# Kernel optimization log

Measured on AMD Instinct MI355X. Metric: run time of the kernel, lower is better.

Reference implementation:

```python
import jax, jax.numpy as jnp
import numpy as np

HIDDEN = 2048
N_HEADS = 32
N_KV_HEADS = 8
HEAD_DIM = 64
MAX_SEQ_LEN = 4096
ROPE_THETA = 500000.0
B, L = 1, 2048
EPS = 1e-6
NEG = -1e9


def precompute_rope(head_dim, max_seq_len, theta):
    freqs = 1.0 / theta ** (jnp.arange(0, head_dim, 2, dtype=jnp.float32) / head_dim)
    pos = jnp.arange(max_seq_len, dtype=jnp.float32)
    ang = pos[:, None] * freqs[None, :]                     # [S, hd/2]
    cos = jnp.repeat(jnp.cos(ang), 2, axis=-1)              # [S, hd]
    sin = jnp.repeat(jnp.sin(ang), 2, axis=-1)
    return cos, sin


def apply_rope(x, cos, sin):
    # x: [B, H, L, hd]; interleaved (even/odd) rotation, faithful to torch code
    seq_len = x.shape[2]
    c = cos[:seq_len][None, None, :, ::2]                   # [1,1,L,hd/2]
    s = sin[:seq_len][None, None, :, ::2]
    x1 = x[..., ::2]
    x2 = x[..., 1::2]
    o1 = x1 * c - x2 * s
    o2 = x2 * c + x1 * s
    return jnp.stack([o1, o2], axis=-1).reshape(x.shape)


def rmsnorm(x, w):
    return x * jax.lax.rsqrt(jnp.mean(x * x, axis=-1, keepdims=True) + EPS) * w


def setup_inputs() -> dict:
    key = jax.random.key(0)
    ks = jax.random.split(key, 6)
    x = jax.random.normal(ks[0], (B, L, HIDDEN), dtype=jnp.float32)
    causal = jnp.tril(jnp.ones((L, L), dtype=bool))
    mask = jnp.where(causal, 0.0, NEG).astype(jnp.float32)  # additive causal mask
    scale = 0.02
    norm_w = jnp.ones((HIDDEN,), dtype=jnp.float32)
    Wq = jax.random.normal(ks[1], (N_HEADS * HEAD_DIM, HIDDEN), dtype=jnp.float32) * scale
    Wk = jax.random.normal(ks[2], (N_KV_HEADS * HEAD_DIM, HIDDEN), dtype=jnp.float32) * scale
    Wv = jax.random.normal(ks[3], (N_KV_HEADS * HEAD_DIM, HIDDEN), dtype=jnp.float32) * scale
    Wo = jax.random.normal(ks[4], (HIDDEN, N_HEADS * HEAD_DIM), dtype=jnp.float32) * scale
    rope_cos, rope_sin = precompute_rope(HEAD_DIM, MAX_SEQ_LEN, ROPE_THETA)
    return {"x": x, "mask": mask, "norm_w": norm_w, "Wq": Wq, "Wk": Wk,
            "Wv": Wv, "Wo": Wo, "rope_cos": rope_cos, "rope_sin": rope_sin}


def reference(x, mask, norm_w, Wq, Wk, Wv, Wo, rope_cos, rope_sin):
    Bb, Ll, _ = x.shape
    residual = x
    h = rmsnorm(x, norm_w)
    q = (h @ Wq.T).reshape(Bb, Ll, N_HEADS, HEAD_DIM).transpose(0, 2, 1, 3)     # [B,H,L,hd]
    k = (h @ Wk.T).reshape(Bb, Ll, N_KV_HEADS, HEAD_DIM).transpose(0, 2, 1, 3)  # [B,Hk,L,hd]
    v = (h @ Wv.T).reshape(Bb, Ll, N_KV_HEADS, HEAD_DIM).transpose(0, 2, 1, 3)
    q = apply_rope(q, rope_cos, rope_sin)
    k = apply_rope(k, rope_cos, rope_sin)
    n_groups = N_HEADS // N_KV_HEADS
    if n_groups > 1:
        k = jnp.repeat(k, n_groups, axis=1)   # GQA repeat_interleave
        v = jnp.repeat(v, n_groups, axis=1)
    scale = jnp.sqrt(jnp.asarray(HEAD_DIM, dtype=q.dtype))
    attn = jnp.einsum('bhld,bhmd->bhlm', q, k) / scale
    attn = attn + mask                                       # broadcast [L,L]
    attn = jax.nn.softmax(attn, axis=-1)
    out = jnp.einsum('bhlm,bhmd->bhld', attn, v)
    out = out.transpose(0, 2, 1, 3).reshape(Bb, Ll, N_HEADS * HEAD_DIM)
    return out @ Wo.T + residual
```

## Files before the change

### kernel.cpp

```cpp
#include <hip/hip_runtime.h>
#include <stdint.h>

#define L_SEQ 2048
#define HID   2048
#define NHEAD 32
#define NKV   8
#define HD    64
#define KVDIM 512
#define QSCALE 0.18033688f

typedef __attribute__((ext_vector_type(8))) short s16x8;
typedef __attribute__((ext_vector_type(4))) short s16x4;
typedef __attribute__((ext_vector_type(4))) float f32x4;

__device__ __forceinline__ short f2bf(float f) {
  __bf16 b = (__bf16)f;
  short s;
  __builtin_memcpy(&s, &b, 2);
  return s;
}

__device__ __forceinline__ void gload16(const void* g, void* l) {
  __builtin_amdgcn_global_load_lds(
      (const __attribute__((address_space(1))) void*)g,
      (__attribute__((address_space(3))) void*)l, 16, 0, 0);
}

__global__ __launch_bounds__(256) void pre_kernel(
    const float* __restrict__ x, const float* __restrict__ w,
    const float* __restrict__ wq, const float* __restrict__ wk,
    const float* __restrict__ wv, const float* __restrict__ wo,
    short* __restrict__ h,
    short* __restrict__ owq, short* __restrict__ owk,
    short* __restrict__ owv, short* __restrict__ owo) {
  const int tid = threadIdx.x;
  if (blockIdx.x >= 2048) {
    int64_t e = ((int64_t)(blockIdx.x - 2048) * 256 + tid) * 4;
    const float* src; short* dst; int64_t o;
    if (e < 4194304)      { src = wq; dst = owq; o = e; }
    else if (e < 5242880) { src = wk; dst = owk; o = e - 4194304; }
    else if (e < 6291456) { src = wv; dst = owv; o = e - 5242880; }
    else                  { src = wo; dst = owo; o = e - 6291456; }
    f32x4 v = *(const f32x4*)(src + o);
    s16x4 b;
    b[0] = f2bf(v[0]); b[1] = f2bf(v[1]); b[2] = f2bf(v[2]); b[3] = f2bf(v[3]);
    *(s16x4*)(dst + o) = b;
    return;
  }
  const int row = blockIdx.x;
  const float* xr = x + (int64_t)row * HID + tid * 8;
  f32x4 a = *(const f32x4*)(xr);
  f32x4 b = *(const f32x4*)(xr + 4);
  float ss = a[0]*a[0]+a[1]*a[1]+a[2]*a[2]+a[3]*a[3]
           + b[0]*b[0]+b[1]*b[1]+b[2]*b[2]+b[3]*b[3];
  #pragma unroll
  for (int off = 1; off < 64; off <<= 1) ss += __shfl_xor(ss, off, 64);
  __shared__ float sred[4];
  if ((tid & 63) == 0) sred[tid >> 6] = ss;
  __syncthreads();
  const float scale = rsqrtf((sred[0]+sred[1]+sred[2]+sred[3]) * (1.0f/HID) + 1e-6f);
  const float* wp = w + tid * 8;
  f32x4 wa = *(const f32x4*)(wp);
  f32x4 wb = *(const f32x4*)(wp + 4);
  s16x8 o;
  o[0]=f2bf(a[0]*scale*wa[0]); o[1]=f2bf(a[1]*scale*wa[1]);
  o[2]=f2bf(a[2]*scale*wa[2]); o[3]=f2bf(a[3]*scale*wa[3]);
  o[4]=f2bf(b[0]*scale*wb[0]); o[5]=f2bf(b[1]*scale*wb[1]);
  o[6]=f2bf(b[2]*scale*wb[2]); o[7]=f2bf(b[3]*scale*wb[3]);
  *(s16x8*)(h + (int64_t)row * HID + tid * 8) = o;
}

__device__ __forceinline__ void gemm_core_128x64(
    const short* __restrict__ A, const short* __restrict__ B,
    short* sA, short* sB, f32x4 acc[4][2]) {
  const int tid = threadIdx.x;
  const int lane = tid & 63;
  const int w = tid >> 6, wr = w >> 1, wc = w & 1;
  const int g = lane >> 4, li = lane & 15;

  auto stage = [&](int k0, int buf) {
    #pragma unroll
    for (int i = 0; i < 4; ++i) {
      const int flat = i * 256 + tid;
      const int row = flat >> 3, c8 = flat & 7;
      const int sc = c8 ^ (row & 7);
      gload16(A + (int64_t)row * HID + k0 + sc * 8, sA + buf * 8192 + flat * 8);
    }
    #pragma unroll
    for (int i = 0; i < 2; ++i) {
      const int flat = i * 256 + tid;
      const int row = flat >> 3, c8 = flat & 7;
      const int sc = c8 ^ (row & 7);
      gload16(B + (int64_t)row * HID + k0 + sc * 8, sB + buf * 4096 + flat * 8);
    }
  };

  stage(0, 0);
  for (int k0 = 0; k0 < HID; k0 += 64) {
    const int cur = (k0 >> 6) & 1;
    __syncthreads();
    if (k0 + 64 < HID) stage(k0 + 64, cur ^ 1);
    const short* cA = sA + cur * 8192;
    const short* cB = sB + cur * 4096;
    #pragma unroll
    for (int kk = 0; kk < 2; ++kk) {
      s16x8 af[4], bfr[2];
      const int chunk = (kk << 2) | g;
      #pragma unroll
      for (int m = 0; m < 4; ++m) {
        const int row = wr * 64 + m * 16 + li;
        af[m] = *(const s16x8*)(cA + row * 64 + ((chunk ^ (li & 7)) << 3));
      }
      #pragma unroll
      for (int n = 0; n < 2; ++n) {
        const int row = wc * 32 + n * 16 + li;
        bfr[n] = *(const s16x8*)(cB + row * 64 + ((chunk ^ (li & 7)) << 3));
      }
      __builtin_amdgcn_s_setprio(1);
      #pragma unroll
      for (int m = 0; m < 4; ++m)
        #pragma unroll
        for (int n = 0; n < 2; ++n)
          acc[m][n] = __builtin_amdgcn_mfma_f32_16x16x32_bf16(af[m], bfr[n], acc[m][n], 0, 0, 0);
      __builtin_amdgcn_s_setprio(0);
    }
  }
}

__global__ __launch_bounds__(256) void qkv_kernel(
    const short* __restrict__ h16, const short* __restrict__ wq,
    const short* __restrict__ wk, const short* __restrict__ wv,
    short* __restrict__ qo, short* __restrict__ ko, short* __restrict__ vto,
    const float* __restrict__ rc, const float* __restrict__ rs) {
  __shared__ short sA[2 * 128 * 64];
  __shared__ short sB[2 * 64 * 64];
  const int cb = blockIdx.x, rb = blockIdx.y;
  const short* B; short* out; int colbase, mode; int64_t ldc;
  if (cb < 32)      { B = wq + (int64_t)cb * 64 * HID;        out = qo;  colbase = cb * 64;        mode = 0; ldc = HID;   }
  else if (cb < 40) { B = wk + (int64_t)(cb - 32) * 64 * HID; out = ko;  colbase = (cb - 32) * 64; mode = 0; ldc = KVDIM; }
  else              { B = wv + (int64_t)(cb - 40) * 64 * HID; out = vto; colbase = (cb - 40) * 64; mode = 1; ldc = L_SEQ; }
  const float rsc = (cb < 32) ? QSCALE : 1.0f;

  f32x4 acc[4][2];
  const f32x4 z = {0.f, 0.f, 0.f, 0.f};
  #pragma unroll
  for (int m = 0; m < 4; ++m)
    #pragma unroll
    for (int n = 0; n < 2; ++n) acc[m][n] = z;

  gemm_core_128x64(h16 + (int64_t)rb * 128 * HID, B, sA, sB, acc);

  const int lane = threadIdx.x & 63;
  const int w = threadIdx.x >> 6, wr = w >> 1, wc = w & 1;
  const int g = lane >> 4, li = lane & 15;

  if (mode == 0) {
    #pragma unroll
    for (int m = 0; m < 4; ++m) {
      #pragma unroll
      for (int n = 0; n < 2; ++n) {
        const int col = colbase + wc * 32 + n * 16 + li;
        const int d2 = col & 62;
        #pragma unroll
        for (int r = 0; r < 4; ++r) {
          const int row = rb * 128 + wr * 64 + m * 16 + g * 4 + r;
          const float c = rc[row * 64 + d2] * rsc;
          const float s = rs[row * 64 + d2] * rsc;
          const float v0 = acc[m][n][r];
          const float pr = __shfl_xor(v0, 1, 64);
          const float o = (lane & 1) ? (v0 * c + pr * s) : (v0 * c - pr * s);
          out[(int64_t)row * ldc + col] = f2bf(o);
        }
      }
    }
  } else {
    #pragma unroll
    for (int m = 0; m < 4; ++m) {
      #pragma unroll
      for (int n = 0; n < 2; ++n) {
        const int col = colbase + wc * 32 + n * 16 + li;
        const int row0 = rb * 128 + wr * 64 + m * 16 + g * 4;
        s16x4 pk;
        pk[0] = f2bf(acc[m][n][0]); pk[1] = f2bf(acc[m][n][1]);
        pk[2] = f2bf(acc[m][n][2]); pk[3] = f2bf(acc[m][n][3]);
        *(s16x4*)(out + (int64_t)col * L_SEQ + row0) = pk;
      }
    }
  }
}

__global__ __launch_bounds__(512, 4) void attn_kernel(
    const short* __restrict__ q16, const short* __restrict__ k16,
    const short* __restrict__ vt16, short* __restrict__ out16) {
  __shared__ short sK[2 * 64 * 64];
  __shared__ short sV[2 * 64 * 64];
  __shared__ short sP[8][16 * 64];
  const int pi = blockIdx.x, h = blockIdx.y, kvh = h >> 2;
  const int qbL = pi, qbH = 31 - pi;
  const int tid = threadIdx.x, lane = tid & 63, w = tid >> 6, wl = w & 3;
  const int g = lane >> 4, li = lane & 15;
  const int myqb = (w < 4) ? qbL : qbH;
  short* sPw = &sP[w][0];

  s16x8 qf[2];
  {
    const int qr = myqb * 64 + wl * 16 + li;
    #pragma unroll
    for (int kk = 0; kk < 2; ++kk)
      qf[kk] = *(const s16x8*)(q16 + (int64_t)qr * HID + h * 64 + kk * 32 + g * 8);
  }

  f32x4 acc[4];
  const f32x4 z = {0.f, 0.f, 0.f, 0.f};
  #pragma unroll
  for (int n = 0; n < 4; ++n) acc[n] = z;
  float m = -1e30f, l = 0.f;

  auto stage = [&](int t, int buf) {
    const int kv0 = t * 64;
    const int row = tid >> 3, c8 = tid & 7;
    const int sc = c8 ^ (row & 7);
    gload16(k16 + (int64_t)(kv0 + row) * KVDIM + kvh * 64 + sc * 8,
            sK + buf * 4096 + tid * 8);
    gload16(vt16 + (int64_t)(kvh * 64 + row) * L_SEQ + kv0 + sc * 8,
            sV + buf * 4096 + tid * 8);
  };

  stage(0, 0);
  for (int t = 0; t <= qbH; ++t) {
    const int cur = t & 1;
    __syncthreads();
    if (t < qbH) stage(t + 1, cur ^ 1);
    if (w >= 4 || t <= qbL) {
      const short* cK = sK + cur * 4096;
      const short* cV = sV + cur * 4096;

      s16x8 kf[2][4];
      #pragma unroll
      for (int kk = 0; kk < 2; ++kk)
        #pragma unroll
        for (int n = 0; n < 4; ++n)
          kf[kk][n] = *(const s16x8*)(cK + (n * 16 + li) * 64 + ((((kk << 2) | g) ^ (li & 7)) << 3));
      f32x4 s[4];
      #pragma unroll
      for (int n = 0; n < 4; ++n) s[n] = z;
      __builtin_amdgcn_s_setprio(1);
      #pragma unroll
      for (int kk = 0; kk < 2; ++kk)
        #pragma unroll
        for (int n = 0; n < 4; ++n)
          s[n] = __builtin_amdgcn_mfma_f32_16x16x32_bf16(kf[kk][n], qf[kk], s[n], 0, 0, 0);
      __builtin_amdgcn_s_setprio(0);

      if (t == myqb) {
        const int ql = wl * 16 + li;
        #pragma unroll
        for (int n = 0; n < 4; ++n)
          #pragma unroll
          for (int r = 0; r < 4; ++r)
            if (n * 16 + g * 4 + r > ql) s[n][r] = -1e30f;
      }

      float mx = fmaxf(fmaxf(s[0][0], s[0][1]), fmaxf(s[0][2], s[0][3]));
      #pragma unroll
      for (int n = 1; n < 4; ++n)
        mx = fmaxf(mx, fmaxf(fmaxf(s[n][0], s[n][1]), fmaxf(s[n][2], s[n][3])));
      mx = fmaxf(mx, __shfl_xor(mx, 16, 64));
      mx = fmaxf(mx, __shfl_xor(mx, 32, 64));
      if (__any(mx > m + 8.0f)) {
        const float mn = fmaxf(m, mx);
        const float al = __builtin_amdgcn_exp2f(m - mn);
        m = mn;
        l *= al;
        #pragma unroll
        for (int dt = 0; dt < 4; ++dt)
          #pragma unroll
          for (int r = 0; r < 4; ++r) acc[dt][r] *= al;
      }
      float ps = 0.f;
      #pragma unroll
      for (int n = 0; n < 4; ++n) {
        s16x4 pk;
        #pragma unroll
        for (int r = 0; r < 4; ++r) {
          const float p = __builtin_amdgcn_exp2f(s[n][r] - m);
          pk[r] = f2bf(p);
          ps += p;
        }
        *(s16x4*)(sPw + li * 64 + (((n * 2 + (g >> 1)) ^ (li & 7)) << 3) + (g & 1) * 4) = pk;
      }
      ps += __shfl_xor(ps, 16, 64);
      ps += __shfl_xor(ps, 32, 64);
      l += ps;

      s16x8 vf[2][4];
      #pragma unroll
      for (int kk = 0; kk < 2; ++kk)
        #pragma unroll
        for (int dt = 0; dt < 4; ++dt)
          vf[kk][dt] = *(const s16x8*)(cV + (dt * 16 + li) * 64 + ((((kk << 2) | g) ^ (li & 7)) << 3));
      #pragma unroll
      for (int kk = 0; kk < 2; ++kk) {
        s16x8 pf = *(const s16x8*)(sPw + li * 64 + (((kk * 4 + g) ^ (li & 7)) << 3));
        __builtin_amdgcn_s_setprio(1);
        #pragma unroll
        for (int dt = 0; dt < 4; ++dt)
          acc[dt] = __builtin_amdgcn_mfma_f32_16x16x32_bf16(vf[kk][dt], pf, acc[dt], 0, 0, 0);
        __builtin_amdgcn_s_setprio(0);
      }
    }
  }

  const float rl = 1.0f / l;
  #pragma unroll
  for (int n2 = 0; n2 < 4; ++n2) {
    s16x4 o;
    #pragma unroll
    for (int r = 0; r < 4; ++r) o[r] = f2bf(acc[n2][r] * rl);
    *(s16x4*)(sPw + li * 64 + (((n2 * 2 + (g >> 1)) ^ (li & 7)) << 3) + (g & 1) * 4) = o;
  }
  #pragma unroll
  for (int half = 0; half < 2; ++half) {
    const int chunk = half * 64 + lane;
    const int q = chunk >> 3, c = chunk & 7;
    s16x8 v = *(const s16x8*)(sPw + q * 64 + ((c ^ (q & 7)) << 3));
    *(s16x8*)(out16 + (int64_t)(myqb * 64 + wl * 16 + q) * HID + h * 64 + c * 8) = v;
  }
}

__global__ __launch_bounds__(256) void oproj_kernel(
    const short* __restrict__ ao, const short* __restrict__ wo,
    const float* __restrict__ resid, float* __restrict__ out) {
  __shared__ short sA[2 * 128 * 64];
  __shared__ short sB[2 * 64 * 64];
  const int cb = blockIdx.x, rb = blockIdx.y;
  f32x4 acc[4][2];
  const f32x4 z = {0.f, 0.f, 0.f, 0.f};
  #pragma unroll
  for (int m = 0; m < 4; ++m)
    #pragma unroll
    for (int n = 0; n < 2; ++n) acc[m][n] = z;

  gemm_core_128x64(ao + (int64_t)rb * 128 * HID, wo + (int64_t)cb * 64 * HID, sA, sB, acc);

  const int lane = threadIdx.x & 63;
  const int w = threadIdx.x >> 6, wr = w >> 1, wc = w & 1;
  const int g = lane >> 4, li = lane & 15;
  #pragma unroll
  for (int m = 0; m < 4; ++m) {
    #pragma unroll
    for (int n = 0; n < 2; ++n) {
      const int col = cb * 64 + wc * 32 + n * 16 + li;
      #pragma unroll
      for (int r = 0; r < 4; ++r) {
        const int row = rb * 128 + wr * 64 + m * 16 + g * 4 + r;
        out[(int64_t)row * HID + col] = acc[m][n][r] + resid[(int64_t)row * HID + col];
      }
    }
  }
}

extern "C" void kernel_launch(void* const* d_in, const int* in_sizes, int n_in,
                              void* d_out, int out_size, void* d_ws, size_t ws_size,
                              hipStream_t stream) {
  (void)in_sizes; (void)n_in; (void)out_size; (void)ws_size;
  const float* x      = (const float*)d_in[0];
  const float* norm_w = (const float*)d_in[2];
  const float* Wq     = (const float*)d_in[3];
  const float* Wk     = (const float*)d_in[4];
  const float* Wv     = (const float*)d_in[5];
  const float* Wo     = (const float*)d_in[6];
  const float* rc     = (const float*)d_in[7];
  const float* rs     = (const float*)d_in[8];
  float* out = (float*)d_out;

  char* ws = (char*)d_ws;
  short* wq16 = (short*)(ws);
  short* wk16 = (short*)(ws + 8388608);
  short* wv16 = (short*)(ws + 10485760);
  short* wo16 = (short*)(ws + 12582912);
  short* h16  = (short*)(ws + 20971520);
  short* q16  = (short*)(ws + 29360128);
  short* k16  = (short*)(ws + 37748736);
  short* vt16 = (short*)(ws + 39845888);
  short* ao16 = (short*)(ws + 41943040);

  pre_kernel<<<12288, 256, 0, stream>>>(x, norm_w, Wq, Wk, Wv, Wo,
                                        h16, wq16, wk16, wv16, wo16);
  qkv_kernel<<<dim3(48, 16), 256, 0, stream>>>(h16, wq16, wk16, wv16, q16, k16, vt16, rc, rs);
  attn_kernel<<<dim3(16, NHEAD), 512, 0, stream>>>(q16, k16, vt16, ao16);
  oproj_kernel<<<dim3(32, 16), 256, 0, stream>>>(ao16, wo16, x, out);
}
```

Baseline: 127.3 us.

## Process four query blocks per attention workgroup to reuse staged K/V tiles

Each attention workgroup now handles four causal query blocks (two per wave group: kb/31-kb and 8+kb/23-kb) instead of two, and the grid is halved to 8x32. Each K/V tile staged into LDS and loaded into registers is shared by two query blocks per wave, which cuts LDS staging and global K/V traffic per unit of work. In exchange there are half as many workgroups (256 on a large GPU), more registers per wave for the extra accumulators and Q fragments, and possible load imbalance between the two wave groups.

```diff
diff --git a/kernel.cpp b/kernel.cpp
--- a/kernel.cpp
+++ b/kernel.cpp
@@ -189,32 +189,111 @@
   }
 }
 
+__device__ __forceinline__ void softmax_pv(
+    f32x4 s[4], const s16x8 vf[2][4], bool diag,
+    int w, int g, int li, short* sPw,
+    float& m, float& l, f32x4 acc[4]) {
+  if (diag) {
+    const int ql = w * 16 + li;
+    #pragma unroll
+    for (int n = 0; n < 4; ++n)
+      #pragma unroll
+      for (int r = 0; r < 4; ++r)
+        if (n * 16 + g * 4 + r > ql) s[n][r] = -1e30f;
+  }
+  float mx = fmaxf(fmaxf(s[0][0], s[0][1]), fmaxf(s[0][2], s[0][3]));
+  #pragma unroll
+  for (int n = 1; n < 4; ++n)
+    mx = fmaxf(mx, fmaxf(fmaxf(s[n][0], s[n][1]), fmaxf(s[n][2], s[n][3])));
+  mx = fmaxf(mx, __shfl_xor(mx, 16, 64));
+  mx = fmaxf(mx, __shfl_xor(mx, 32, 64));
+  if (__any(mx > m + 8.0f)) {
+    const float mn = fmaxf(m, mx);
+    const float al = __builtin_amdgcn_exp2f(m - mn);
+    m = mn;
+    l *= al;
+    #pragma unroll
+    for (int dt = 0; dt < 4; ++dt)
+      #pragma unroll
+      for (int r = 0; r < 4; ++r) acc[dt][r] *= al;
+  }
+  float ps = 0.f;
+  #pragma unroll
+  for (int n = 0; n < 4; ++n) {
+    s16x4 pk;
+    #pragma unroll
+    for (int r = 0; r < 4; ++r) {
+      const float p = __builtin_amdgcn_exp2f(s[n][r] - m);
+      pk[r] = f2bf(p);
+      ps += p;
+    }
+    *(s16x4*)(sPw + li * 64 + (((n * 2 + (g >> 1)) ^ (li & 7)) << 3) + (g & 1) * 4) = pk;
+  }
+  ps += __shfl_xor(ps, 16, 64);
+  ps += __shfl_xor(ps, 32, 64);
+  l += ps;
+  #pragma unroll
+  for (int kk = 0; kk < 2; ++kk) {
+    s16x8 pf = *(const s16x8*)(sPw + li * 64 + (((kk * 4 + g) ^ (li & 7)) << 3));
+    __builtin_amdgcn_s_setprio(1);
+    #pragma unroll
+    for (int dt = 0; dt < 4; ++dt)
+      acc[dt] = __builtin_amdgcn_mfma_f32_16x16x32_bf16(vf[kk][dt], pf, acc[dt], 0, 0, 0);
+    __builtin_amdgcn_s_setprio(0);
+  }
+}
+
+__device__ __forceinline__ void write_out(
+    const f32x4 acc[4], float l, int qb, int h, int w, int g, int li, int lane,
+    short* sPw, short* __restrict__ out16) {
+  const float rl = 1.0f / l;
+  #pragma unroll
+  for (int n2 = 0; n2 < 4; ++n2) {
+    s16x4 o;
+    #pragma unroll
+    for (int r = 0; r < 4; ++r) o[r] = f2bf(acc[n2][r] * rl);
+    *(s16x4*)(sPw + li * 64 + (((n2 * 2 + (g >> 1)) ^ (li & 7)) << 3) + (g & 1) * 4) = o;
+  }
+  #pragma unroll
+  for (int half = 0; half < 2; ++half) {
+    const int chunk = half * 64 + lane;
+    const int q = chunk >> 3, c = chunk & 7;
+    s16x8 v = *(const s16x8*)(sPw + q * 64 + ((c ^ (q & 7)) << 3));
+    *(s16x8*)(out16 + (int64_t)(qb * 64 + w * 16 + q) * HID + h * 64 + c * 8) = v;
+  }
+}
+
 __global__ __launch_bounds__(512, 4) void attn_kernel(
     const short* __restrict__ q16, const short* __restrict__ k16,
     const short* __restrict__ vt16, short* __restrict__ out16) {
   __shared__ short sK[2 * 64 * 64];
   __shared__ short sV[2 * 64 * 64];
   __shared__ short sP[8][16 * 64];
-  const int pi = blockIdx.x, h = blockIdx.y, kvh = h >> 2;
-  const int qbL = pi, qbH = 31 - pi;
+  const int kb = blockIdx.x;
+  const int h = blockIdx.y, kvh = h >> 2;
   const int tid = threadIdx.x, lane = tid & 63, w = tid >> 6, wl = w & 3;
   const int g = lane >> 4, li = lane & 15;
-  const int myqb = (w < 4) ? qbL : qbH;
+  const int myqbL = (w < 4) ? kb : 8 + kb;
+  const int myqbH = (w < 4) ? 31 - kb : 23 - kb;
+  const int tmax = 31 - kb;
   short* sPw = &sP[w][0];
 
-  s16x8 qf[2];
+  s16x8 qfL[2], qfH[2];
   {
-    const int qr = myqb * 64 + wl * 16 + li;
-    #pragma unroll
-    for (int kk = 0; kk < 2; ++kk)
-      qf[kk] = *(const s16x8*)(q16 + (int64_t)qr * HID + h * 64 + kk * 32 + g * 8);
-  }
-
-  f32x4 acc[4];
+    const int qrL = myqbL * 64 + wl * 16 + li;
+    const int qrH = myqbH * 64 + wl * 16 + li;
+    #pragma unroll
+    for (int kk = 0; kk < 2; ++kk) {
+      qfL[kk] = *(const s16x8*)(q16 + (int64_t)qrL * HID + h * 64 + kk * 32 + g * 8);
+      qfH[kk] = *(const s16x8*)(q16 + (int64_t)qrH * HID + h * 64 + kk * 32 + g * 8);
+    }
+  }
+
+  f32x4 accL[4], accH[4];
   const f32x4 z = {0.f, 0.f, 0.f, 0.f};
   #pragma unroll
-  for (int n = 0; n < 4; ++n) acc[n] = z;
-  float m = -1e30f, l = 0.f;
+  for (int n = 0; n < 4; ++n) { accL[n] = z; accH[n] = z; }
+  float mL = -1e30f, lL = 0.f, mH = -1e30f, lH = 0.f;
 
   auto stage = [&](int t, int buf) {
     const int kv0 = t * 64;
@@ -227,11 +306,13 @@
   };
 
   stage(0, 0);
-  for (int t = 0; t <= qbH; ++t) {
+  for (int t = 0; t <= tmax; ++t) {
     const int cur = t & 1;
     __syncthreads();
-    if (t < qbH) stage(t + 1, cur ^ 1);
-    if (w >= 4 || t <= qbL) {
+    if (t < tmax) stage(t + 1, cur ^ 1);
+    const bool doH = (t <= myqbH);
+    const bool doL = (t <= myqbL);
+    if (doH) {
       const short* cK = sK + cur * 4096;
       const short* cV = sV + cur * 4096;
 
@@ -241,57 +322,28 @@
         #pragma unroll
         for (int n = 0; n < 4; ++n)
           kf[kk][n] = *(const s16x8*)(cK + (n * 16 + li) * 64 + ((((kk << 2) | g) ^ (li & 7)) << 3));
-      f32x4 s[4];
-      #pragma unroll
-      for (int n = 0; n < 4; ++n) s[n] = z;
+
+      f32x4 sH[4], sL[4];
+      #pragma unroll
+      for (int n = 0; n < 4; ++n) sH[n] = z;
       __builtin_amdgcn_s_setprio(1);
       #pragma unroll
       for (int kk = 0; kk < 2; ++kk)
         #pragma unroll
         for (int n = 0; n < 4; ++n)
-          s[n] = __builtin_amdgcn_mfma_f32_16x16x32_bf16(kf[kk][n], qf[kk], s[n], 0, 0, 0);
+          sH[n] = __builtin_amdgcn_mfma_f32_16x16x32_bf16(kf[kk][n], qfH[kk], sH[n], 0, 0, 0);
       __builtin_amdgcn_s_setprio(0);
-
-      if (t == myqb) {
-        const int ql = wl * 16 + li;
-        #pragma unroll
-        for (int n = 0; n < 4; ++n)
+      if (doL) {
+        #pragma unroll
+        for (int n = 0; n < 4; ++n) sL[n] = z;
+        __builtin_amdgcn_s_setprio(1);
+        #pragma unroll
+        for (int kk = 0; kk < 2; ++kk)
           #pragma unroll
-          for (int r = 0; r < 4; ++r)
-            if (n * 16 + g * 4 + r > ql) s[n][r] = -1e30f;
-      }
-
-      float mx = fmaxf(fmaxf(s[0][0], s[0][1]), fmaxf(s[0][2], s[0][3]));
-      #pragma unroll
-      for (int n = 1; n < 4; ++n)
-        mx = fmaxf(mx, fmaxf(fmaxf(s[n][0], s[n][1]), fmaxf(s[n][2], s[n][3])));
-      mx = fmaxf(mx, __shfl_xor(mx, 16, 64));
-      mx = fmaxf(mx, __shfl_xor(mx, 32, 64));
-      if (__any(mx > m + 8.0f)) {
-        const float mn = fmaxf(m, mx);
-        const float al = __builtin_amdgcn_exp2f(m - mn);
-        m = mn;
-        l *= al;
-        #pragma unroll
-        for (int dt = 0; dt < 4; ++dt)
-          #pragma unroll
-          for (int r = 0; r < 4; ++r) acc[dt][r] *= al;
-      }
-      float ps = 0.f;
-      #pragma unroll
-      for (int n = 0; n < 4; ++n) {
-        s16x4 pk;
-        #pragma unroll
-        for (int r = 0; r < 4; ++r) {
-          const float p = __builtin_amdgcn_exp2f(s[n][r] - m);
-          pk[r] = f2bf(p);
-          ps += p;
-        }
-        *(s16x4*)(sPw + li * 64 + (((n * 2 + (g >> 1)) ^ (li & 7)) << 3) + (g & 1) * 4) = pk;
-      }
-      ps += __shfl_xor(ps, 16, 64);
-      ps += __shfl_xor(ps, 32, 64);
-      l += ps;
+          for (int n = 0; n < 4; ++n)
+            sL[n] = __builtin_amdgcn_mfma_f32_16x16x32_bf16(kf[kk][n], qfL[kk], sL[n], 0, 0, 0);
+        __builtin_amdgcn_s_setprio(0);
+      }
 
       s16x8 vf[2][4];
       #pragma unroll
@@ -299,33 +351,14 @@
         #pragma unroll
         for (int dt = 0; dt < 4; ++dt)
           vf[kk][dt] = *(const s16x8*)(cV + (dt * 16 + li) * 64 + ((((kk << 2) | g) ^ (li & 7)) << 3));
-      #pragma unroll
-      for (int kk = 0; kk < 2; ++kk) {
-        s16x8 pf = *(const s16x8*)(sPw + li * 64 + (((kk * 4 + g) ^ (li & 7)) << 3));
-        __builtin_amdgcn_s_setprio(1);
-        #pragma unroll
-        for (int dt = 0; dt < 4; ++dt)
-          acc[dt] = __builtin_amdgcn_mfma_f32_16x16x32_bf16(vf[kk][dt], pf, acc[dt], 0, 0, 0);
-        __builtin_amdgcn_s_setprio(0);
-      }
-    }
-  }
-
-  const float rl = 1.0f / l;
-  #pragma unroll
-  for (int n2 = 0; n2 < 4; ++n2) {
-    s16x4 o;
-    #pragma unroll
-    for (int r = 0; r < 4; ++r) o[r] = f2bf(acc[n2][r] * rl);
-    *(s16x4*)(sPw + li * 64 + (((n2 * 2 + (g >> 1)) ^ (li & 7)) << 3) + (g & 1) * 4) = o;
-  }
-  #pragma unroll
-  for (int half = 0; half < 2; ++half) {
-    const int chunk = half * 64 + lane;
-    const int q = chunk >> 3, c = chunk & 7;
-    s16x8 v = *(const s16x8*)(sPw + q * 64 + ((c ^ (q & 7)) << 3));
-    *(s16x8*)(out16 + (int64_t)(myqb * 64 + wl * 16 + q) * HID + h * 64 + c * 8) = v;
-  }
+
+      softmax_pv(sH, vf, t == myqbH, wl, g, li, sPw, mH, lH, accH);
+      if (doL) softmax_pv(sL, vf, t == myqbL, wl, g, li, sPw, mL, lL, accL);
+    }
+  }
+
+  write_out(accL, lL, myqbL, h, wl, g, li, lane, sPw, out16);
+  write_out(accH, lH, myqbH, h, wl, g, li, lane, sPw, out16);
 }
 
 __global__ __launch_bounds__(256) void oproj_kernel(
@@ -388,6 +421,6 @@
   pre_kernel<<<12288, 256, 0, stream>>>(x, norm_w, Wq, Wk, Wv, Wo,
                                         h16, wq16, wk16, wv16, wo16);
   qkv_kernel<<<dim3(48, 16), 256, 0, stream>>>(h16, wq16, wk16, wv16, q16, k16, vt16, rc, rs);
-  attn_kernel<<<dim3(16, NHEAD), 512, 0, stream>>>(q16, k16, vt16, ao16);
+  attn_kernel<<<dim3(8, NHEAD), 512, 0, stream>>>(q16, k16, vt16, ao16);
   oproj_kernel<<<dim3(32, 16), 256, 0, stream>>>(ao16, wo16, x, out);
 }
```

After: 154.9 us. 1.22x slower.

## Process two KV tiles per barrier with doubled LDS staging in attention

Applied to the files above, without the earlier changes.

The attention loop now stages two 64-row K/V tiles per iteration into a 4-slot LDS buffer and processes both before the next barrier. This halves the number of __syncthreads calls and gives larger prefetch batches. In exchange LDS use per block roughly doubles (K/V grows from 32KB to 64KB), which may reduce occupancy below the launch-bounds target. There is also a redundant load when the tile count is odd.

```diff
diff --git a/kernel.cpp b/kernel.cpp
--- a/kernel.cpp
+++ b/kernel.cpp
@@ -192,8 +192,8 @@
 __global__ __launch_bounds__(512, 4) void attn_kernel(
     const short* __restrict__ q16, const short* __restrict__ k16,
     const short* __restrict__ vt16, short* __restrict__ out16) {
-  __shared__ short sK[2 * 64 * 64];
-  __shared__ short sV[2 * 64 * 64];
+  __shared__ short sK[4 * 64 * 64];
+  __shared__ short sV[4 * 64 * 64];
   __shared__ short sP[8][16 * 64];
   const int pi = blockIdx.x, h = blockIdx.y, kvh = h >> 2;
   const int qbL = pi, qbH = 31 - pi;
@@ -216,97 +216,107 @@
   for (int n = 0; n < 4; ++n) acc[n] = z;
   float m = -1e30f, l = 0.f;
 
-  auto stage = [&](int t, int buf) {
+  auto stage1 = [&](int t, int buf, int slot) {
     const int kv0 = t * 64;
     const int row = tid >> 3, c8 = tid & 7;
     const int sc = c8 ^ (row & 7);
+    const int off = (buf * 2 + slot) * 4096;
     gload16(k16 + (int64_t)(kv0 + row) * KVDIM + kvh * 64 + sc * 8,
-            sK + buf * 4096 + tid * 8);
+            sK + off + tid * 8);
     gload16(vt16 + (int64_t)(kvh * 64 + row) * L_SEQ + kv0 + sc * 8,
-            sV + buf * 4096 + tid * 8);
+            sV + off + tid * 8);
   };
 
-  stage(0, 0);
-  for (int t = 0; t <= qbH; ++t) {
-    const int cur = t & 1;
+  stage1(0, 0, 0);
+  stage1(1, 0, 1);
+  for (int tp = 0; 2 * tp <= qbH; ++tp) {
+    const int buf = tp & 1;
     __syncthreads();
-    if (t < qbH) stage(t + 1, cur ^ 1);
-    if (w >= 4 || t <= qbL) {
-      const short* cK = sK + cur * 4096;
-      const short* cV = sV + cur * 4096;
-
-      s16x8 kf[2][4];
-      #pragma unroll
-      for (int kk = 0; kk < 2; ++kk)
-        #pragma unroll
-        for (int n = 0; n < 4; ++n)
-          kf[kk][n] = *(const s16x8*)(cK + (n * 16 + li) * 64 + ((((kk << 2) | g) ^ (li & 7)) << 3));
-      f32x4 s[4];
-      #pragma unroll
-      for (int n = 0; n < 4; ++n) s[n] = z;
-      __builtin_amdgcn_s_setprio(1);
-      #pragma unroll
-      for (int kk = 0; kk < 2; ++kk)
-        #pragma unroll
-        for (int n = 0; n < 4; ++n)
-          s[n] = __builtin_amdgcn_mfma_f32_16x16x32_bf16(kf[kk][n], qf[kk], s[n], 0, 0, 0);
-      __builtin_amdgcn_s_setprio(0);
-
-      if (t == myqb) {
-        const int ql = wl * 16 + li;
-        #pragma unroll
-        for (int n = 0; n < 4; ++n)
-          #pragma unroll
-          for (int r = 0; r < 4; ++r)
-            if (n * 16 + g * 4 + r > ql) s[n][r] = -1e30f;
-      }
-
-      float mx = fmaxf(fmaxf(s[0][0], s[0][1]), fmaxf(s[0][2], s[0][3]));
-      #pragma unroll
-      for (int n = 1; n < 4; ++n)
-        mx = fmaxf(mx, fmaxf(fmaxf(s[n][0], s[n][1]), fmaxf(s[n][2], s[n][3])));
-      mx = fmaxf(mx, __shfl_xor(mx, 16, 64));
-      mx = fmaxf(mx, __shfl_xor(mx, 32, 64));
-      if (__any(mx > m + 8.0f)) {
-        const float mn = fmaxf(m, mx);
-        const float al = __builtin_amdgcn_exp2f(m - mn);
-        m = mn;
-        l *= al;
-        #pragma unroll
-        for (int dt = 0; dt < 4; ++dt)
-          #pragma unroll
-          for (int r = 0; r < 4; ++r) acc[dt][r] *= al;
-      }
-      float ps = 0.f;
-      #pragma unroll
-      for (int n = 0; n < 4; ++n) {
-        s16x4 pk;
-        #pragma unroll
-        for (int r = 0; r < 4; ++r) {
-          const float p = __builtin_amdgcn_exp2f(s[n][r] - m);
-          pk[r] = f2bf(p);
-          ps += p;
+    if (2 * tp + 2 <= qbH) {
+      stage1(2 * tp + 2, buf ^ 1, 0);
+      const int t3 = 2 * tp + 3;
+      stage1(t3 <= qbH ? t3 : t3 - 1, buf ^ 1, 1);
+    }
+    #pragma unroll
+    for (int sl = 0; sl < 2; ++sl) {
+      const int t = 2 * tp + sl;
+      if (t <= qbH && (w >= 4 || t <= qbL)) {
+        const short* cK = sK + (buf * 2 + sl) * 4096;
+        const short* cV = sV + (buf * 2 + sl) * 4096;
+
+        s16x8 kf[2][4];
+        #pragma unroll
+        for (int kk = 0; kk < 2; ++kk)
+          #pragma unroll
+          for (int n = 0; n < 4; ++n)
+            kf[kk][n] = *(const s16x8*)(cK + (n * 16 + li) * 64 + ((((kk << 2) | g) ^ (li & 7)) << 3));
+        f32x4 s[4];
+        #pragma unroll
+        for (int n = 0; n < 4; ++n) s[n] = z;
+        __builtin_amdgcn_s_setprio(1);
+        #pragma unroll
+        for (int kk = 0; kk < 2; ++kk)
+          #pragma unroll
+          for (int n = 0; n < 4; ++n)
+            s[n] = __builtin_amdgcn_mfma_f32_16x16x32_bf16(kf[kk][n], qf[kk], s[n], 0, 0, 0);
+        __builtin_amdgcn_s_setprio(0);
+
+        if (t == myqb) {
+          const int ql = wl * 16 + li;
+          #pragma unroll
+          for (int n = 0; n < 4; ++n)
+            #pragma unroll
+            for (int r = 0; r < 4; ++r)
+              if (n * 16 + g * 4 + r > ql) s[n][r] = -1e30f;
         }
-        *(s16x4*)(sPw + li * 64 + (((n * 2 + (g >> 1)) ^ (li & 7)) << 3) + (g & 1) * 4) = pk;
-      }
-      ps += __shfl_xor(ps, 16, 64);
-      ps += __shfl_xor(ps, 32, 64);
-      l += ps;
-
-      s16x8 vf[2][4];
-      #pragma unroll
-      for (int kk = 0; kk < 2; ++kk)
-        #pragma unroll
-        for (int dt = 0; dt < 4; ++dt)
-          vf[kk][dt] = *(const s16x8*)(cV + (dt * 16 + li) * 64 + ((((kk << 2) | g) ^ (li & 7)) << 3));
-      #pragma unroll
-      for (int kk = 0; kk < 2; ++kk) {
-        s16x8 pf = *(const s16x8*)(sPw + li * 64 + (((kk * 4 + g) ^ (li & 7)) << 3));
-        __builtin_amdgcn_s_setprio(1);
-        #pragma unroll
-        for (int dt = 0; dt < 4; ++dt)
-          acc[dt] = __builtin_amdgcn_mfma_f32_16x16x32_bf16(vf[kk][dt], pf, acc[dt], 0, 0, 0);
-        __builtin_amdgcn_s_setprio(0);
+
+        float mx = fmaxf(fmaxf(s[0][0], s[0][1]), fmaxf(s[0][2], s[0][3]));
+        #pragma unroll
+        for (int n = 1; n < 4; ++n)
+          mx = fmaxf(mx, fmaxf(fmaxf(s[n][0], s[n][1]), fmaxf(s[n][2], s[n][3])));
+        mx = fmaxf(mx, __shfl_xor(mx, 16, 64));
+        mx = fmaxf(mx, __shfl_xor(mx, 32, 64));
+        if (__any(mx > m + 8.0f)) {
+          const float mn = fmaxf(m, mx);
+          const float al = __builtin_amdgcn_exp2f(m - mn);
+          m = mn;
+          l *= al;
+          #pragma unroll
+          for (int dt = 0; dt < 4; ++dt)
+            #pragma unroll
+            for (int r = 0; r < 4; ++r) acc[dt][r] *= al;
+        }
+        float ps = 0.f;
+        #pragma unroll
+        for (int n = 0; n < 4; ++n) {
+          s16x4 pk;
+          #pragma unroll
+          for (int r = 0; r < 4; ++r) {
+            const float p = __builtin_amdgcn_exp2f(s[n][r] - m);
+            pk[r] = f2bf(p);
+            ps += p;
+          }
+          *(s16x4*)(sPw + li * 64 + (((n * 2 + (g >> 1)) ^ (li & 7)) << 3) + (g & 1) * 4) = pk;
+        }
+        ps += __shfl_xor(ps, 16, 64);
+        ps += __shfl_xor(ps, 32, 64);
+        l += ps;
+
+        s16x8 vf[2][4];
+        #pragma unroll
+        for (int kk = 0; kk < 2; ++kk)
+          #pragma unroll
+          for (int dt = 0; dt < 4; ++dt)
+            vf[kk][dt] = *(const s16x8*)(cV + (dt * 16 + li) * 64 + ((((kk << 2) | g) ^ (li & 7)) << 3));
+        #pragma unroll
+        for (int kk = 0; kk < 2; ++kk) {
+          s16x8 pf = *(const s16x8*)(sPw + li * 64 + (((kk * 4 + g) ^ (li & 7)) << 3));
+          __builtin_amdgcn_s_setprio(1);
+          #pragma unroll
+          for (int dt = 0; dt < 4; ++dt)
+            acc[dt] = __builtin_amdgcn_mfma_f32_16x16x32_bf16(vf[kk][dt], pf, acc[dt], 0, 0, 0);
+          __builtin_amdgcn_s_setprio(0);
+        }
       }
     }
   }
```

Result: faster. 124.1 us (-2.4%).
